# Kernel tuning notes

Hardware: AMD Instinct MI355X
Metric: run time of the kernel (lower is better)

The kernel has to match this reference:

```python
import jax, jax.numpy as jnp
import numpy as np

ALL_WINDOW_SIZES = [1, 2, 4, 8, 16, 32]
ATTENTION_WINDOW = 32
T, D, N = 8192, 128, 4096
NW = len(ALL_WINDOW_SIZES)


def _layernorm(x, g, b, eps=1e-5):
    mu = x.mean(axis=-1, keepdims=True)
    var = ((x - mu) ** 2).mean(axis=-1, keepdims=True)
    return (x - mu) / jnp.sqrt(var + eps) * g + b


def setup_inputs() -> dict:
    key = jax.random.key(0)
    ks = jax.random.split(key, 16)
    s = 0.02
    return {
        "inputEmbeds": jax.random.normal(ks[0], (T, D), dtype=jnp.float32),
        # per-neuron weights stacked -> Linear(D, N)
        "neuronW": jax.random.normal(ks[1], (D, N), dtype=jnp.float32) * s,
        "neuronB": jnp.zeros((N,), dtype=jnp.float32),
        # tiny attention layer (single head, Q/K/V projections)
        "Wq": jax.random.normal(ks[2], (D, D), dtype=jnp.float32) * s,
        "bq": jnp.zeros((D,), dtype=jnp.float32),
        "Wk": jax.random.normal(ks[3], (D, D), dtype=jnp.float32) * s,
        "bk": jnp.zeros((D,), dtype=jnp.float32),
        "Wv": jax.random.normal(ks[4], (D, D), dtype=jnp.float32) * s,
        "bv": jnp.zeros((D,), dtype=jnp.float32),
        # attentionProjection = LayerNorm(D) -> Linear(D, N)
        "ln_g": jnp.ones((D,), dtype=jnp.float32),
        "ln_b": jnp.zeros((D,), dtype=jnp.float32),
        "projW": jax.random.normal(ks[5], (D, N), dtype=jnp.float32) * s,
        "projb": jnp.zeros((N,), dtype=jnp.float32),
        "windowWeighting": jnp.ones((NW,), dtype=jnp.float32),
        # combinationLayer: Linear(N*NW, N)
        "comboW": jax.random.normal(ks[6], (N * NW, N), dtype=jnp.float32) * 0.005,
        "combob": jnp.zeros((N,), dtype=jnp.float32),
    }


def _tiny_attn(x, Wq, bq, Wk, bk, Wv, bv):
    # x: [B, W, D] -> single-head self attention
    q = x @ Wq + bq
    k = x @ Wk + bk
    v = x @ Wv + bv
    scores = jnp.einsum("bqd,bkd->bqk", q, k) / jnp.sqrt(jnp.asarray(x.shape[-1], x.dtype))
    return jnp.einsum("bqk,bkd->bqd", jax.nn.softmax(scores, axis=-1), v)


def reference(inputEmbeds, neuronW, neuronB, Wq, bq, Wk, bk, Wv, bv,
              ln_g, ln_b, projW, projb, windowWeighting, comboW, combob):
    # all neurons over all tokens: [T, N], tanh activation, clamp to [-5, 5]
    acts = jnp.clip(jnp.tanh(inputEmbeds @ neuronW + neuronB), -5.0, 5.0)

    window_means = []
    for w in ALL_WINDOW_SIZES:
        if w == ATTENTION_WINDOW:
            xw = inputEmbeds[-w:][None]  # [1, w, D]
            attended = _tiny_attn(xw, Wq, bq, Wk, bk, Wv, bv)  # [1, w, D]
            attn_mean = attended.mean(axis=1)  # [1, D]
            proj = _layernorm(attn_mean, ln_g, ln_b) @ projW + projb  # [1, N]
            window_means.append(proj)
        else:
            window_means.append(acts[-w:].mean(axis=0, keepdims=True))  # [1, N]

    norm_w = (windowWeighting + 0.1) / (windowWeighting.sum() + 0.1)
    weighted = jnp.concatenate(
        [window_means[i] * norm_w[i] for i in range(NW)], axis=1)  # [1, N*NW]
    return weighted @ comboW + combob  # [1, N]
```

## Files before the change

### kernel.cpp

```cpp
#include <hip/hip_runtime.h>

#define T_TOK 8192
#define D_DIM 128
#define N_NEU 4096
#define RPC 96
#define NCHUNK 256

typedef float f4_t __attribute__((ext_vector_type(4)));

struct SmemActs {
    float xs16[16][128];
    float wst[32][256];
};
struct SmemQkv {
    float xs[32][128];
    float w[128][128];
};
union SmemA {
    SmemActs a;
    SmemQkv q;
};

__global__ void acts_qkv_kernel(
    const float* __restrict__ x,
    const float* __restrict__ neuronW, const float* __restrict__ neuronB,
    const float* __restrict__ Wq, const float* __restrict__ bq,
    const float* __restrict__ Wk, const float* __restrict__ bk,
    const float* __restrict__ Wv, const float* __restrict__ bv,
    float* __restrict__ means,
    float* __restrict__ qkv)
{
    __shared__ SmemA sm;
    const int tid = threadIdx.x;
    const int bid = blockIdx.x;

    if (bid < 16) {
        const int n0 = bid * 256;
        const int n = n0 + tid;
        for (int idx = tid; idx < 16 * 128; idx += 256) {
            int t = idx >> 7, d = idx & 127;
            sm.a.xs16[t][d] = x[(size_t)(T_TOK - 16 + t) * D_DIM + d];
        }
        float acc[16];
        float bias = neuronB[n];
#pragma unroll
        for (int t = 0; t < 16; ++t) acc[t] = bias;
        const f4_t* W4 = reinterpret_cast<const f4_t*>(neuronW);
        f4_t* wst4 = reinterpret_cast<f4_t*>(&sm.a.wst[0][0]);
        for (int c = 0; c < 4; ++c) {
            const int d0 = c * 32;
            __syncthreads();
#pragma unroll
            for (int k = 0; k < 8; ++k) {
                int idx = tid + k * 256;
                int dd = idx >> 6, j4 = idx & 63;
                wst4[dd * 64 + j4] = W4[(size_t)(d0 + dd) * 1024 + (n0 >> 2) + j4];
            }
            __syncthreads();
#pragma unroll
            for (int dd = 0; dd < 32; ++dd) {
                float w = sm.a.wst[dd][tid];
#pragma unroll
                for (int t = 0; t < 16; ++t) acc[t] += sm.a.xs16[t][d0 + dd] * w;
            }
        }
#pragma unroll
        for (int t = 0; t < 16; ++t) acc[t] = tanhf(acc[t]);
        float s1 = acc[15];
        float s2 = s1 + acc[14];
        float s4 = s2 + acc[13] + acc[12];
        float s8 = s4 + acc[11] + acc[10] + acc[9] + acc[8];
        float s16 = s8 + acc[7] + acc[6] + acc[5] + acc[4] + acc[3] + acc[2] + acc[1] + acc[0];
        means[0 * N_NEU + n] = s1;
        means[1 * N_NEU + n] = s2 * 0.5f;
        means[2 * N_NEU + n] = s4 * 0.25f;
        means[3 * N_NEU + n] = s8 * 0.125f;
        means[4 * N_NEU + n] = s16 * 0.0625f;
        return;
    }

    const int m = bid - 16;
    const float* Wm = (m == 0) ? Wq : ((m == 1) ? Wk : Wv);
    const float* bb = (m == 0) ? bq : ((m == 1) ? bk : bv);

    f4_t* xs4 = reinterpret_cast<f4_t*>(&sm.q.xs[0][0]);
    const f4_t* X4 = reinterpret_cast<const f4_t*>(x + (size_t)(T_TOK - 32) * D_DIM);
#pragma unroll
    for (int k = 0; k < 4; ++k) xs4[tid + k * 256] = X4[tid + k * 256];
    f4_t* w4 = reinterpret_cast<f4_t*>(&sm.q.w[0][0]);
    const f4_t* Wm4 = reinterpret_cast<const f4_t*>(Wm);
#pragma unroll
    for (int k = 0; k < 16; ++k) w4[tid + k * 256] = Wm4[tid + k * 256];
    __syncthreads();

    const int d = tid & 127;
    const int g = tid >> 7;
    float acc[16];
    float bias = bb[d];
#pragma unroll
    for (int i = 0; i < 16; ++i) acc[i] = bias;
#pragma unroll 4
    for (int e = 0; e < 128; ++e) {
        float w = sm.q.w[e][d];
#pragma unroll
        for (int i = 0; i < 16; ++i) acc[i] += sm.q.xs[g * 16 + i][e] * w;
    }
#pragma unroll
    for (int i = 0; i < 16; ++i) qkv[m * 4096 + (g * 16 + i) * 128 + d] = acc[i];
}

struct SmemAttn {
    float qs[32][128];
    float kt[128][33];
    float vs[32][128];
    float ps[32][33];
    float pbar[32];
    float mvec[128];
    float red[2];
};

__global__ void attn_kernel(const float* __restrict__ qkv,
                            const float* __restrict__ ln_g, const float* __restrict__ ln_b,
                            float* __restrict__ yvec)
{
    __shared__ SmemAttn sm;
    const int tid = threadIdx.x;
    for (int idx = tid; idx < 32 * 128; idx += 256) {
        int i = idx >> 7, d = idx & 127;
        sm.qs[i][d] = qkv[idx];
        sm.kt[d][i] = qkv[4096 + idx];
        sm.vs[i][d] = qkv[8192 + idx];
    }
    __syncthreads();
    const float scale = 0.08838834764831845f;
#pragma unroll
    for (int rep = 0; rep < 4; ++rep) {
        int idx = tid + rep * 256;
        int i = idx >> 5, j = idx & 31;
        float acc = 0.f;
        for (int e = 0; e < 128; ++e) acc += sm.qs[i][e] * sm.kt[e][j];
        sm.ps[i][j] = acc * scale;
    }
    __syncthreads();
    if (tid < 32) {
        float mx = -1e30f;
        for (int j = 0; j < 32; ++j) mx = fmaxf(mx, sm.ps[tid][j]);
        float s = 0.f;
        for (int j = 0; j < 32; ++j) { float e = expf(sm.ps[tid][j] - mx); sm.ps[tid][j] = e; s += e; }
        float inv = 1.f / s;
        for (int j = 0; j < 32; ++j) sm.ps[tid][j] *= inv;
    }
    __syncthreads();
    if (tid < 32) {
        float s = 0.f;
        for (int i = 0; i < 32; ++i) s += sm.ps[i][tid];
        sm.pbar[tid] = s * (1.f / 32.f);
    }
    __syncthreads();
    if (tid < 128) {
        float s = 0.f;
        for (int j = 0; j < 32; ++j) s += sm.pbar[j] * sm.vs[j][tid];
        sm.mvec[tid] = s;
    }
    __syncthreads();
    if (tid < 64) {
        float p = sm.mvec[tid] + sm.mvec[tid + 64];
        for (int off = 32; off; off >>= 1) p += __shfl_down(p, off);
        if (tid == 0) sm.red[0] = p * (1.f / 128.f);
    }
    __syncthreads();
    float mu = sm.red[0];
    if (tid < 64) {
        float t1 = sm.mvec[tid] - mu, t2 = sm.mvec[tid + 64] - mu;
        float p = t1 * t1 + t2 * t2;
        for (int off = 32; off; off >>= 1) p += __shfl_down(p, off);
        if (tid == 0) sm.red[1] = rsqrtf(p * (1.f / 128.f) + 1e-5f);
    }
    __syncthreads();
    if (tid < 128) {
        yvec[tid] = (sm.mvec[tid] - mu) * sm.red[1] * ln_g[tid] + ln_b[tid];
    }
}

__global__ __launch_bounds__(1024) void combo_partial_kernel(
    const float* __restrict__ means,
    const float* __restrict__ ww,
    const float* __restrict__ yvec,
    const float* __restrict__ projW,
    const float* __restrict__ projb,
    const float* __restrict__ comboW,
    float* __restrict__ part)
{
    __shared__ float vsm[RPC];
    __shared__ float ys[128];
    const int tid = threadIdx.x;
    const int chunk = blockIdx.x;
    const int row0 = chunk * RPC;

    if (tid < 128) ys[tid] = yvec[tid];
    float denom = 0.1f;
#pragma unroll
    for (int i = 0; i < 6; ++i) denom += ww[i];
    __syncthreads();

    if (tid < RPC) {
        int r = row0 + tid;
        int seg = r >> 12;
        int m = r & 4095;
        float nw = (ww[seg] + 0.1f) / denom;
        float val;
        if (seg < 5) {
            val = means[seg * N_NEU + m];
        } else {
            float acc = projb[m];
#pragma unroll 4
            for (int e = 0; e < 128; ++e) acc += ys[e] * projW[e * N_NEU + m];
            val = acc;
        }
        vsm[tid] = val * nw;
    }
    __syncthreads();

    const f4_t* W4 = reinterpret_cast<const f4_t*>(comboW);
    const size_t base = (size_t)row0 * 1024 + tid;
    f4_t acc = {0.f, 0.f, 0.f, 0.f};
#pragma unroll 8
    for (int r = 0; r < RPC; ++r) {
        float v = vsm[r];
        f4_t w = W4[base + (size_t)r * 1024];
        acc += w * v;
    }
    reinterpret_cast<f4_t*>(part)[(size_t)chunk * 1024 + tid] = acc;
}

__global__ void combo_reduce_kernel(const float* __restrict__ part,
                                    const float* __restrict__ bias,
                                    float* __restrict__ out)
{
    __shared__ f4_t red[4][64];
    const int tid = threadIdx.x;
    const int h = tid >> 6;
    const int j = tid & 63;
    const int n4 = blockIdx.x * 64 + j;
    const f4_t* P4 = reinterpret_cast<const f4_t*>(part);
    f4_t acc = {0.f, 0.f, 0.f, 0.f};
#pragma unroll 8
    for (int c = h * 64; c < h * 64 + 64; ++c)
        acc += P4[(size_t)c * 1024 + n4];
    red[h][j] = acc;
    __syncthreads();
    if (h == 0) {
        f4_t s = red[0][j] + red[1][j] + red[2][j] + red[3][j];
        s += reinterpret_cast<const f4_t*>(bias)[n4];
        reinterpret_cast<f4_t*>(out)[n4] = s;
    }
}

extern "C" void kernel_launch(void* const* d_in, const int* in_sizes, int n_in,
                              void* d_out, int out_size, void* d_ws, size_t ws_size,
                              hipStream_t stream) {
    const float* inputEmbeds = (const float*)d_in[0];
    const float* neuronW     = (const float*)d_in[1];
    const float* neuronB     = (const float*)d_in[2];
    const float* Wq          = (const float*)d_in[3];
    const float* bq          = (const float*)d_in[4];
    const float* Wk          = (const float*)d_in[5];
    const float* bk          = (const float*)d_in[6];
    const float* Wv          = (const float*)d_in[7];
    const float* bv          = (const float*)d_in[8];
    const float* ln_g        = (const float*)d_in[9];
    const float* ln_b        = (const float*)d_in[10];
    const float* projW       = (const float*)d_in[11];
    const float* projb       = (const float*)d_in[12];
    const float* ww          = (const float*)d_in[13];
    const float* comboW      = (const float*)d_in[14];
    const float* combob      = (const float*)d_in[15];
    float* out = (float*)d_out;
    float* ws  = (float*)d_ws;

    float* means = ws;
    float* yvec  = ws + 20480;
    float* part  = ws + 20608;
    float* qkv   = ws + 20608 + NCHUNK * 4096;

    acts_qkv_kernel<<<19, 256, 0, stream>>>(inputEmbeds, neuronW, neuronB,
                                            Wq, bq, Wk, bk, Wv, bv, means, qkv);
    attn_kernel<<<1, 256, 0, stream>>>(qkv, ln_g, ln_b, yvec);
    combo_partial_kernel<<<NCHUNK, 1024, 0, stream>>>(means, ww, yvec,
                                                      projW, projb, comboW, part);
    combo_reduce_kernel<<<16, 256, 0, stream>>>(part, combob, out);
}
```

Baseline: 131.0 us.

## Precompute weighted combo input vector in separate kernel and split GEMV finer

Moves construction of the weighted concatenated vector (window means plus the projected attention vector) into a new build_v kernel that stages projW through shared memory with coalesced loads. Before, a few combo blocks each ran a serial 128-step GEMV with strided loads, stalling the whole grid. The combo GEMV now uses 2048 blocks of 256 threads over 48 rows each instead of 256 blocks of 1024 threads over 96 rows, raising parallelism over the comboW stream. In exchange it adds a kernel launch and doubles the partial buffer that the reduce kernel has to read.

```diff
diff --git a/kernel.cpp b/kernel.cpp
--- a/kernel.cpp
+++ b/kernel.cpp
@@ -3,8 +3,9 @@
 #define T_TOK 8192
 #define D_DIM 128
 #define N_NEU 4096
-#define RPC 96
-#define NCHUNK 256
+#define RPC 48
+#define NCHUNK 512
+#define NPART NCHUNK
 
 typedef float f4_t __attribute__((ext_vector_type(4)));
 
@@ -182,55 +183,75 @@
     }
 }
 
-__global__ __launch_bounds__(1024) void combo_partial_kernel(
-    const float* __restrict__ means,
-    const float* __restrict__ ww,
-    const float* __restrict__ yvec,
-    const float* __restrict__ projW,
-    const float* __restrict__ projb,
+struct SmemV {
+    float ys[128];
+    float wst[32][256];
+};
+
+__global__ void build_v_kernel(const float* __restrict__ yvec,
+                               const float* __restrict__ projW,
+                               const float* __restrict__ projb,
+                               const float* __restrict__ ww,
+                               const float* __restrict__ means,
+                               float* __restrict__ v)
+{
+    __shared__ SmemV sm;
+    const int tid = threadIdx.x;
+    const int n0 = blockIdx.x * 256;
+    const int n = n0 + tid;
+
+    if (tid < 128) sm.ys[tid] = yvec[tid];
+    float denom = 0.1f;
+#pragma unroll
+    for (int i = 0; i < 6; ++i) denom += ww[i];
+    const float inv = 1.f / denom;
+
+    float acc = projb[n];
+    const f4_t* P4 = reinterpret_cast<const f4_t*>(projW);
+    f4_t* wst4 = reinterpret_cast<f4_t*>(&sm.wst[0][0]);
+    for (int c = 0; c < 4; ++c) {
+        const int d0 = c * 32;
+        __syncthreads();
+#pragma unroll
+        for (int k = 0; k < 8; ++k) {
+            int idx = tid + k * 256;
+            int dd = idx >> 6, j4 = idx & 63;
+            wst4[dd * 64 + j4] = P4[(size_t)(d0 + dd) * 1024 + (n0 >> 2) + j4];
+        }
+        __syncthreads();
+#pragma unroll
+        for (int dd = 0; dd < 32; ++dd) {
+            acc += sm.ys[d0 + dd] * sm.wst[dd][tid];
+        }
+    }
+#pragma unroll
+    for (int s = 0; s < 5; ++s)
+        v[s * N_NEU + n] = means[s * N_NEU + n] * ((ww[s] + 0.1f) * inv);
+    v[5 * N_NEU + n] = acc * ((ww[5] + 0.1f) * inv);
+}
+
+__global__ __launch_bounds__(256) void combo_partial_kernel(
+    const float* __restrict__ v,
     const float* __restrict__ comboW,
     float* __restrict__ part)
 {
     __shared__ float vsm[RPC];
-    __shared__ float ys[128];
-    const int tid = threadIdx.x;
-    const int chunk = blockIdx.x;
+    const int tid = threadIdx.x;
+    const int chunk = blockIdx.x >> 2;
+    const int cb = blockIdx.x & 3;
     const int row0 = chunk * RPC;
 
-    if (tid < 128) ys[tid] = yvec[tid];
-    float denom = 0.1f;
-#pragma unroll
-    for (int i = 0; i < 6; ++i) denom += ww[i];
-    __syncthreads();
-
-    if (tid < RPC) {
-        int r = row0 + tid;
-        int seg = r >> 12;
-        int m = r & 4095;
-        float nw = (ww[seg] + 0.1f) / denom;
-        float val;
-        if (seg < 5) {
-            val = means[seg * N_NEU + m];
-        } else {
-            float acc = projb[m];
-#pragma unroll 4
-            for (int e = 0; e < 128; ++e) acc += ys[e] * projW[e * N_NEU + m];
-            val = acc;
-        }
-        vsm[tid] = val * nw;
-    }
+    if (tid < RPC) vsm[tid] = v[row0 + tid];
     __syncthreads();
 
     const f4_t* W4 = reinterpret_cast<const f4_t*>(comboW);
-    const size_t base = (size_t)row0 * 1024 + tid;
+    const size_t base = (size_t)row0 * 1024 + cb * 256 + tid;
     f4_t acc = {0.f, 0.f, 0.f, 0.f};
 #pragma unroll 8
     for (int r = 0; r < RPC; ++r) {
-        float v = vsm[r];
-        f4_t w = W4[base + (size_t)r * 1024];
-        acc += w * v;
-    }
-    reinterpret_cast<f4_t*>(part)[(size_t)chunk * 1024 + tid] = acc;
+        acc += W4[base + (size_t)r * 1024] * vsm[r];
+    }
+    reinterpret_cast<f4_t*>(part)[(size_t)chunk * 1024 + cb * 256 + tid] = acc;
 }
 
 __global__ void combo_reduce_kernel(const float* __restrict__ part,
@@ -245,7 +266,7 @@
     const f4_t* P4 = reinterpret_cast<const f4_t*>(part);
     f4_t acc = {0.f, 0.f, 0.f, 0.f};
 #pragma unroll 8
-    for (int c = h * 64; c < h * 64 + 64; ++c)
+    for (int c = h * 128; c < h * 128 + 128; ++c)
         acc += P4[(size_t)c * 1024 + n4];
     red[h][j] = acc;
     __syncthreads();
@@ -280,13 +301,14 @@
 
     float* means = ws;
     float* yvec  = ws + 20480;
-    float* part  = ws + 20608;
-    float* qkv   = ws + 20608 + NCHUNK * 4096;
+    float* qkv   = ws + 20608;
+    float* v     = ws + 32896;
+    float* part  = ws + 57472;
 
     acts_qkv_kernel<<<19, 256, 0, stream>>>(inputEmbeds, neuronW, neuronB,
                                             Wq, bq, Wk, bk, Wv, bv, means, qkv);
     attn_kernel<<<1, 256, 0, stream>>>(qkv, ln_g, ln_b, yvec);
-    combo_partial_kernel<<<NCHUNK, 1024, 0, stream>>>(means, ww, yvec,
-                                                      projW, projb, comboW, part);
+    build_v_kernel<<<16, 256, 0, stream>>>(yvec, projW, projb, ww, means, v);
+    combo_partial_kernel<<<NCHUNK * 4, 256, 0, stream>>>(v, comboW, part);
     combo_reduce_kernel<<<16, 256, 0, stream>>>(part, combob, out);
 }
```

Measured after the change: 130.9 us. About the same (-0.1%).
